# Kernel optimization log

Measured on AMD Instinct MI355X. Metric: run time of the kernel, lower is better.

## Reference

```python
import jax, jax.numpy as jnp
import numpy as np


def _build_cost_volume(l, r, D):
    """Vectorized equivalent of the 64-iteration shifted slice-write loop.

    cost[:, :C, i, :, w] = l[:, :, :, w]       for w >= i, else 0
    cost[:, C:, i, :, w] = r[:, :, :, w - i]   for w >= i, else 0
    Returns [B, 2C, D, H, W].
    """
    B, C, H, W = l.shape
    d = jnp.arange(D)[:, None]          # [D, 1]
    w = jnp.arange(W)[None, :]          # [1, W]
    mask = (w >= d)[None, None, :, None, :]   # [1, 1, D, 1, W]
    left = jnp.where(mask, l[:, :, None, :, :], 0.0)            # [B, C, D, H, W]
    idx = jnp.clip(w - d, 0, W - 1)                              # [D, W]
    right = r[:, :, :, idx]                                      # [B, C, H, D, W]
    right = jnp.transpose(right, (0, 1, 3, 2, 4))                # [B, C, D, H, W]
    right = jnp.where(mask, right, 0.0)
    return jnp.concatenate([left, right], axis=1)                # [B, 2C, D, H, W]


def setup_inputs() -> dict:
    key = jax.random.key(0)
    k0, k1, k2, k3 = jax.random.split(key, 4)
    shape = (1, 32, 96, 240)  # [B, C_feat, H/3, W/3]
    return {
        "l0": jax.random.normal(k0, shape, dtype=jnp.float32),
        "r0": jax.random.normal(k1, shape, dtype=jnp.float32),
        "l1": jax.random.normal(k2, shape, dtype=jnp.float32),
        "r1": jax.random.normal(k3, shape, dtype=jnp.float32),
        "max_disp": 192,
    }


def reference(l0, r0, l1, r1, max_disp):
    D = max_disp // 3  # 64 disparity levels at 1/3 resolution
    cost0 = _build_cost_volume(l0, r0, D)
    cost1 = _build_cost_volume(l1, r1, D)
    return jnp.stack([cost0, cost1])  # [2, B, 2C, D, H, W]
```

## Files before the change

kernel.cpp:

```cpp
#include <hip/hip_runtime.h>

#define CC   32
#define C2   64
#define DD   64
#define HH   96
#define WW   240
#define W4   60
#define ROWS_PER_BLOCK 16
#define HB   (HH / ROWS_PER_BLOCK)

typedef float vf4 __attribute__((ext_vector_type(4)));

__global__ __launch_bounds__(256) void cost_volume_kernel(
        const float* __restrict__ l0, const float* __restrict__ r0,
        const float* __restrict__ l1, const float* __restrict__ r1,
        float* __restrict__ out) {
    const unsigned b  = blockIdx.x;
    const unsigned hb = b % HB;
    unsigned t = b / HB;
    const unsigned d = t & 63;  t >>= 6;
    const unsigned c = t & 63;
    const unsigned s = t >> 6;

    const unsigned lane = threadIdx.x & 63;
    const unsigned sub  = threadIdx.x >> 6;
    if (lane >= W4) return;
    const unsigned w0 = lane * 4u;

    const float* Lp = s ? l1 : l0;
    const float* Rp = s ? r1 : r0;
    const bool left = (c < CC);
    const float* src = left ? (Lp + (unsigned)(c * HH) * WW)
                            : (Rp + (unsigned)((c - CC) * HH) * WW);

    const bool m0 = (w0 + 0u >= d);
    const bool m1 = (w0 + 1u >= d);
    const bool m2 = (w0 + 2u >= d);
    const bool m3 = (w0 + 3u >= d);

    const unsigned h0 = hb * ROWS_PER_BLOCK + sub;
    const unsigned rowBase = ((s * C2 + c) * DD + d) * HH;
    vf4* o = reinterpret_cast<vf4*>(out);

#pragma unroll
    for (int ri = 0; ri < 4; ++ri) {
        const unsigned h = h0 + (unsigned)ri * 4u;
        const float* row = src + h * (unsigned)WW;
        vf4 v;
        if (left) {
            const vf4 x = *reinterpret_cast<const vf4*>(row + w0);
            v.x = m0 ? x.x : 0.0f;
            v.y = m1 ? x.y : 0.0f;
            v.z = m2 ? x.z : 0.0f;
            v.w = m3 ? x.w : 0.0f;
        } else {
            v.x = m0 ? row[w0 + 0u - d] : 0.0f;
            v.y = m1 ? row[w0 + 1u - d] : 0.0f;
            v.z = m2 ? row[w0 + 2u - d] : 0.0f;
            v.w = m3 ? row[w0 + 3u - d] : 0.0f;
        }
        __builtin_nontemporal_store(v, &o[(rowBase + h) * (unsigned)W4 + lane]);
    }
}

extern "C" void kernel_launch(void* const* d_in, const int* in_sizes, int n_in,
                              void* d_out, int out_size, void* d_ws, size_t ws_size,
                              hipStream_t stream) {
    const float* l0 = (const float*)d_in[0];
    const float* r0 = (const float*)d_in[1];
    const float* l1 = (const float*)d_in[2];
    const float* r1 = (const float*)d_in[3];
    float* out = (float*)d_out;

    const unsigned nBlocks = 2u * C2 * DD * HB;
    hipLaunchKernelGGL(cost_volume_kernel, dim3(nBlocks), dim3(256), 0, stream,
                       l0, r0, l1, r1, out);
}
```

Baseline: 159.5 us.

## Process one full H×W slice per block with flat float4 indexing

Each block now handles an entire (s, c, d) slice of 96×240 floats using 320 threads, each doing 18 float4 stores over a flat contiguous index, in place of 16 rows with 64-lane groups where 4 lanes sat idle. This removes the idle lanes, cuts the block count sixfold and makes the store stream fully contiguous per block. The column index is tracked incrementally and the right-image shift is computed from the flat offset, with clamping so masked elements stay in bounds. Fewer, longer blocks could reduce scheduling overhead but also lower the number of blocks available to fill the GPU.

```diff
diff --git a/kernel.cpp b/kernel.cpp
--- a/kernel.cpp
+++ b/kernel.cpp
@@ -6,60 +6,65 @@
 #define HH   96
 #define WW   240
 #define W4   60
-#define ROWS_PER_BLOCK 16
-#define HB   (HH / ROWS_PER_BLOCK)
+#define F4_PER_SLICE (HH * W4)
+#define THREADS 320
 
 typedef float vf4 __attribute__((ext_vector_type(4)));
 
-__global__ __launch_bounds__(256) void cost_volume_kernel(
+__global__ __launch_bounds__(THREADS) void cost_volume_kernel(
         const float* __restrict__ l0, const float* __restrict__ r0,
         const float* __restrict__ l1, const float* __restrict__ r1,
         float* __restrict__ out) {
-    const unsigned b  = blockIdx.x;
-    const unsigned hb = b % HB;
-    unsigned t = b / HB;
-    const unsigned d = t & 63;  t >>= 6;
-    const unsigned c = t & 63;
-    const unsigned s = t >> 6;
-
-    const unsigned lane = threadIdx.x & 63;
-    const unsigned sub  = threadIdx.x >> 6;
-    if (lane >= W4) return;
-    const unsigned w0 = lane * 4u;
+    const unsigned b = blockIdx.x;
+    const unsigned d = b & 63u;
+    const unsigned c = (b >> 6) & 63u;
+    const unsigned s = b >> 12;
 
     const float* Lp = s ? l1 : l0;
     const float* Rp = s ? r1 : r0;
     const bool left = (c < CC);
-    const float* src = left ? (Lp + (unsigned)(c * HH) * WW)
-                            : (Rp + (unsigned)((c - CC) * HH) * WW);
+    const float* src = left ? (Lp + c * (HH * WW))
+                            : (Rp + (c - CC) * (HH * WW));
 
-    const bool m0 = (w0 + 0u >= d);
-    const bool m1 = (w0 + 1u >= d);
-    const bool m2 = (w0 + 2u >= d);
-    const bool m3 = (w0 + 3u >= d);
+    vf4* o4 = reinterpret_cast<vf4*>(out) + (size_t)b * F4_PER_SLICE;
 
-    const unsigned h0 = hb * ROWS_PER_BLOCK + sub;
-    const unsigned rowBase = ((s * C2 + c) * DD + d) * HH;
-    vf4* o = reinterpret_cast<vf4*>(out);
+    unsigned f  = threadIdx.x;
+    unsigned w4 = f % 60u;
+    const int dd = (int)d;
 
+    if (left) {
+        const vf4* src4 = reinterpret_cast<const vf4*>(src);
 #pragma unroll
-    for (int ri = 0; ri < 4; ++ri) {
-        const unsigned h = h0 + (unsigned)ri * 4u;
-        const float* row = src + h * (unsigned)WW;
-        vf4 v;
-        if (left) {
-            const vf4 x = *reinterpret_cast<const vf4*>(row + w0);
-            v.x = m0 ? x.x : 0.0f;
-            v.y = m1 ? x.y : 0.0f;
-            v.z = m2 ? x.z : 0.0f;
-            v.w = m3 ? x.w : 0.0f;
-        } else {
-            v.x = m0 ? row[w0 + 0u - d] : 0.0f;
-            v.y = m1 ? row[w0 + 1u - d] : 0.0f;
-            v.z = m2 ? row[w0 + 2u - d] : 0.0f;
-            v.w = m3 ? row[w0 + 3u - d] : 0.0f;
+        for (int i = 0; i < 18; ++i) {
+            const int w0 = (int)(w4 * 4u);
+            const vf4 x = src4[f];
+            vf4 v;
+            v.x = (w0 + 0 >= dd) ? x.x : 0.0f;
+            v.y = (w0 + 1 >= dd) ? x.y : 0.0f;
+            v.z = (w0 + 2 >= dd) ? x.z : 0.0f;
+            v.w = (w0 + 3 >= dd) ? x.w : 0.0f;
+            __builtin_nontemporal_store(v, &o4[f]);
+            f += THREADS;
+            w4 += 20u; if (w4 >= 60u) w4 -= 60u;
         }
-        __builtin_nontemporal_store(v, &o[(rowBase + h) * (unsigned)W4 + lane]);
+    } else {
+#pragma unroll
+        for (int i = 0; i < 18; ++i) {
+            const int w0 = (int)(w4 * 4u);
+            const int e  = (int)(f * 4u) - dd;
+            const int e0 = (e + 0 > 0) ? e + 0 : 0;
+            const int e1 = (e + 1 > 0) ? e + 1 : 0;
+            const int e2 = (e + 2 > 0) ? e + 2 : 0;
+            const int e3 = (e + 3 > 0) ? e + 3 : 0;
+            vf4 v;
+            v.x = (w0 + 0 >= dd) ? src[e0] : 0.0f;
+            v.y = (w0 + 1 >= dd) ? src[e1] : 0.0f;
+            v.z = (w0 + 2 >= dd) ? src[e2] : 0.0f;
+            v.w = (w0 + 3 >= dd) ? src[e3] : 0.0f;
+            __builtin_nontemporal_store(v, &o4[f]);
+            f += THREADS;
+            w4 += 20u; if (w4 >= 60u) w4 -= 60u;
+        }
     }
 }
 
@@ -72,7 +77,7 @@
     const float* r1 = (const float*)d_in[3];
     float* out = (float*)d_out;
 
-    const unsigned nBlocks = 2u * C2 * DD * HB;
-    hipLaunchKernelGGL(cost_volume_kernel, dim3(nBlocks), dim3(256), 0, stream,
+    const unsigned nBlocks = 2u * C2 * DD;
+    hipLaunchKernelGGL(cost_volume_kernel, dim3(nBlocks), dim3(THREADS), 0, stream,
                        l0, r0, l1, r1, out);
 }
```

Measured after the change: 162.1 us. No clear change (+1.7%).

## Loop over disparities per thread, reusing loaded input rows across all levels

Applied to the files above, without the earlier changes.

Each block now handles 4 rows of one channel and walks all 64 disparity levels in a loop. The left input is loaded once into registers and reused for every disparity, and the right input is re-read at shifted offsets, mostly from cache. This cuts the number of blocks and the redundant input reads, but each thread writes 64 strided vf4 stores one slice apart. The nontemporal store hint is also replaced with plain stores, which may change cache behaviour on a large write-only output.

```diff
diff --git a/kernel.cpp b/kernel.cpp
--- a/kernel.cpp
+++ b/kernel.cpp
@@ -1,13 +1,13 @@
 #include <hip/hip_runtime.h>
 
 #define CC   32
-#define C2   64
-#define DD   64
 #define HH   96
 #define WW   240
+#define DD   64
 #define W4   60
-#define ROWS_PER_BLOCK 16
-#define HB   (HH / ROWS_PER_BLOCK)
+#define HQ   4
+#define NHQ  (HH / HQ)
+#define SLICE_F4 (HH * W4)
 
 typedef float vf4 __attribute__((ext_vector_type(4)));
 
@@ -15,51 +15,57 @@
         const float* __restrict__ l0, const float* __restrict__ r0,
         const float* __restrict__ l1, const float* __restrict__ r1,
         float* __restrict__ out) {
-    const unsigned b  = blockIdx.x;
-    const unsigned hb = b % HB;
-    unsigned t = b / HB;
-    const unsigned d = t & 63;  t >>= 6;
-    const unsigned c = t & 63;
-    const unsigned s = t >> 6;
+    unsigned b = blockIdx.x;
+    const unsigned hq   = b % NHQ;  b /= NHQ;
+    const unsigned c    = b & (CC - 1u);  b >>= 5;
+    const unsigned half = b & 1u;
+    const unsigned s    = b >> 1;
 
-    const unsigned lane = threadIdx.x & 63;
-    const unsigned sub  = threadIdx.x >> 6;
-    if (lane >= W4) return;
-    const unsigned w0 = lane * 4u;
+    const unsigned tid = threadIdx.x;
+    if (tid >= 240) return;
+    const unsigned r   = tid / 60u;
+    const unsigned col = tid - r * 60u;
+    const unsigned w0  = col * 4u;
 
-    const float* Lp = s ? l1 : l0;
-    const float* Rp = s ? r1 : r0;
-    const bool left = (c < CC);
-    const float* src = left ? (Lp + (unsigned)(c * HH) * WW)
-                            : (Rp + (unsigned)((c - CC) * HH) * WW);
+    const float* img = half ? (s ? r1 : r0) : (s ? l1 : l0);
+    const float* row = img + (c * HH + hq * HQ + r) * WW;
 
-    const bool m0 = (w0 + 0u >= d);
-    const bool m1 = (w0 + 1u >= d);
-    const bool m2 = (w0 + 2u >= d);
-    const bool m3 = (w0 + 3u >= d);
+    const unsigned cout = half * CC + c;
+    size_t of = (size_t)(s * 2u * CC + cout) * DD * SLICE_F4
+              + (size_t)(hq * HQ + r) * W4 + col;
+    vf4* o4 = reinterpret_cast<vf4*>(out);
 
-    const unsigned h0 = hb * ROWS_PER_BLOCK + sub;
-    const unsigned rowBase = ((s * C2 + c) * DD + d) * HH;
-    vf4* o = reinterpret_cast<vf4*>(out);
-
-#pragma unroll
-    for (int ri = 0; ri < 4; ++ri) {
-        const unsigned h = h0 + (unsigned)ri * 4u;
-        const float* row = src + h * (unsigned)WW;
-        vf4 v;
-        if (left) {
-            const vf4 x = *reinterpret_cast<const vf4*>(row + w0);
-            v.x = m0 ? x.x : 0.0f;
-            v.y = m1 ? x.y : 0.0f;
-            v.z = m2 ? x.z : 0.0f;
-            v.w = m3 ? x.w : 0.0f;
-        } else {
-            v.x = m0 ? row[w0 + 0u - d] : 0.0f;
-            v.y = m1 ? row[w0 + 1u - d] : 0.0f;
-            v.z = m2 ? row[w0 + 2u - d] : 0.0f;
-            v.w = m3 ? row[w0 + 3u - d] : 0.0f;
+    if (!half) {
+        const vf4 x = *reinterpret_cast<const vf4*>(row + w0);
+        const int iw0 = (int)w0;
+#pragma unroll 4
+        for (int d = 0; d < DD; ++d) {
+            const int a = iw0 - d;
+            vf4 v;
+            v.x = (a + 0 >= 0) ? x.x : 0.0f;
+            v.y = (a + 1 >= 0) ? x.y : 0.0f;
+            v.z = (a + 2 >= 0) ? x.z : 0.0f;
+            v.w = (a + 3 >= 0) ? x.w : 0.0f;
+            o4[of] = v;
+            of += SLICE_F4;
         }
-        __builtin_nontemporal_store(v, &o[(rowBase + h) * (unsigned)W4 + lane]);
+    } else {
+        const int iw0 = (int)w0;
+#pragma unroll 4
+        for (int d = 0; d < DD; ++d) {
+            const int a = iw0 - d;
+            const int a0 = (a + 0 > 0) ? a + 0 : 0;
+            const int a1 = (a + 1 > 0) ? a + 1 : 0;
+            const int a2 = (a + 2 > 0) ? a + 2 : 0;
+            const int a3 = (a + 3 > 0) ? a + 3 : 0;
+            vf4 v;
+            v.x = (a + 0 >= 0) ? row[a0] : 0.0f;
+            v.y = (a + 1 >= 0) ? row[a1] : 0.0f;
+            v.z = (a + 2 >= 0) ? row[a2] : 0.0f;
+            v.w = (a + 3 >= 0) ? row[a3] : 0.0f;
+            o4[of] = v;
+            of += SLICE_F4;
+        }
     }
 }
 
@@ -72,7 +78,7 @@
     const float* r1 = (const float*)d_in[3];
     float* out = (float*)d_out;
 
-    const unsigned nBlocks = 2u * C2 * DD * HB;
+    const unsigned nBlocks = 2u * 2u * CC * NHQ;
     hipLaunchKernelGGL(cost_volume_kernel, dim3(nBlocks), dim3(256), 0, stream,
                        l0, r0, l1, r1, out);
 }
```

New measurement: 174.6 us. 1.09x slower.
